# Kernel tuning notes

Measured on AMD Instinct MI355X. Metric: run time of the kernel, lower is better.

The kernel has to match this reference:

```python
import jax, jax.numpy as jnp
import numpy as np

IN_CHANNELS = 256


def setup_inputs() -> dict:
    key = jax.random.key(0)
    k0, k1, k2, k3 = jax.random.split(key, 4)
    N, C = 8192, IN_CHANNELS
    x = jax.random.normal(k0, (N, C), dtype=jnp.float32)
    # nn.Linear(C, C, bias=False): y = x @ W.T, W is [out, in] = [C, C]
    s = 1.0 / np.sqrt(C)
    Wq = jax.random.uniform(k1, (C, C), dtype=jnp.float32, minval=-s, maxval=s)
    Wk = jax.random.uniform(k2, (C, C), dtype=jnp.float32, minval=-s, maxval=s)
    Wv = jax.random.uniform(k3, (C, C), dtype=jnp.float32, minval=-s, maxval=s)
    return {"x": x, "Wq": Wq, "Wk": Wk, "Wv": Wv}


def reference(x, Wq, Wk, Wv):
    C = x.shape[-1]
    q = x @ Wq.T  # [N, C]
    k = x @ Wk.T  # [N, C]
    v = x @ Wv.T  # [N, C]
    scores = (q @ k.T) / jnp.sqrt(jnp.asarray(C, dtype=x.dtype))  # [N, N]
    attn = jax.nn.softmax(scores, axis=-1)
    return attn @ v  # [N, C]
```

## Files before the change

kernel.cpp:

```cpp
#include <hip/hip_runtime.h>
#include <hip/hip_bf16.h>


typedef short short8 __attribute__((ext_vector_type(8)));
typedef float f32x4 __attribute__((ext_vector_type(4)));
typedef float f32x16 __attribute__((ext_vector_type(16)));
typedef unsigned int u32x4 __attribute__((ext_vector_type(4)));

#define AS1 __attribute__((address_space(1)))
#define AS3 __attribute__((address_space(3)))

static __device__ __forceinline__ void gl_lds16(const void* g, void* l) {
    __builtin_amdgcn_global_load_lds((const AS1 unsigned int*)g,
                                     (AS3 unsigned int*)l, 16, 0, 0);
}

static __device__ __forceinline__ unsigned short f2bf(float f) {
    __hip_bfloat16 h = __float2bfloat16(f);
    return __builtin_bit_cast(unsigned short, h);
}
static __device__ __forceinline__ float bf2f(unsigned short u) {
    unsigned x = ((unsigned)u) << 16;
    return __builtin_bit_cast(float, x);
}
static __device__ __forceinline__ float exp2_fast(float x) {
    float r; asm("v_exp_f32 %0, %1" : "=v"(r) : "v"(x)); return r;
}
static __device__ __forceinline__ unsigned cvt_pk_bf16(float lo, float hi) {
    unsigned r;
    asm("v_cvt_pk_bf16_f32 %0, %1, %2" : "=v"(r) : "v"(lo), "v"(hi));
    return r;
}

static __device__ __forceinline__ short8 pack8(float4 a, float4 b) {
    short8 v;
    v[0] = (short)f2bf(a.x); v[1] = (short)f2bf(a.y);
    v[2] = (short)f2bf(a.z); v[3] = (short)f2bf(a.w);
    v[4] = (short)f2bf(b.x); v[5] = (short)f2bf(b.y);
    v[6] = (short)f2bf(b.z); v[7] = (short)f2bf(b.w);
    return v;
}

__global__ __launch_bounds__(256) void proj_kernel(
    const float* __restrict__ x, const float* __restrict__ Wq,
    const float* __restrict__ Wk, const float* __restrict__ Wv,
    unsigned short* __restrict__ qb, unsigned short* __restrict__ kbt,
    unsigned short* __restrict__ vtc)
{
    const int mb = blockIdx.x, nb = blockIdx.y;
    __shared__ unsigned short xs[64 * 256];
    __shared__ unsigned short wsh[64 * 256];
    const int tid = threadIdx.x;
    const int wid = tid >> 6, lane = tid & 63;
    const int l15 = lane & 15, kg = lane >> 4;

    for (int i = 0; i < 8; ++i) {
        int id = i * 256 + tid;
        int r = id >> 5, c = id & 31;
        {
            const float* g = x + (size_t)(mb * 64 + r) * 256 + c * 8;
            float4 f0 = *(const float4*)g, f1 = *(const float4*)(g + 4);
            *(short8*)&xs[r * 256 + ((c ^ (r & 7)) * 8)] = pack8(f0, f1);
        }
        {
            const float* g = Wq + (size_t)(nb * 64 + r) * 256 + c * 8;
            float4 f0 = *(const float4*)g, f1 = *(const float4*)(g + 4);
            *(short8*)&wsh[r * 256 + ((c ^ (r & 7)) * 8)] = pack8(f0, f1);
        }
    }
    __syncthreads();

    const int arow = wid * 16 + l15;
    short8 a[8];
#pragma unroll
    for (int ks = 0; ks < 8; ++ks)
        a[ks] = *(const short8*)&xs[arow * 256 + (((ks * 4 + kg) ^ (arow & 7)) * 8)];

    for (int w = 0; w < 3; ++w) {
        const float scale = (w == 0) ? 0.09016844005555f : 1.0f;
#pragma unroll
        for (int nt = 0; nt < 4; ++nt) {
            f32x4 acc = {0.f, 0.f, 0.f, 0.f};
            const int brow = nt * 16 + l15;
#pragma unroll
            for (int ks = 0; ks < 8; ++ks) {
                short8 b = *(const short8*)&wsh[brow * 256 + (((ks * 4 + kg) ^ (brow & 7)) * 8)];
                acc = __builtin_amdgcn_mfma_f32_16x16x32_bf16(a[ks], b, acc, 0, 0, 0);
            }
            const int gcol = nb * 64 + nt * 16 + l15;
#pragma unroll
            for (int r = 0; r < 4; ++r) {
                const int grow = mb * 64 + wid * 16 + kg * 4 + r;
                unsigned short h = f2bf(acc[r] * scale);
                if (w == 0) {
                    qb[(size_t)grow * 256 + gcol] = h;
                } else if (w == 1) {
                    kbt[(size_t)(grow >> 6) * 16384 + (gcol >> 3) * 512
                        + (grow & 63) * 8 + (gcol & 7)] = h;
                } else {
                    vtc[(size_t)(grow >> 3) * 2048 + (size_t)gcol * 8 + (grow & 7)] = h;
                }
            }
        }
        if (w < 2) {
            __syncthreads();
            const float* Wn = (w == 0) ? Wk : Wv;
            for (int i = 0; i < 8; ++i) {
                int id = i * 256 + tid;
                int r = id >> 5, c = id & 31;
                const float* g = Wn + (size_t)(nb * 64 + r) * 256 + c * 8;
                float4 f0 = *(const float4*)g, f1 = *(const float4*)(g + 4);
                *(short8*)&wsh[r * 256 + ((c ^ (r & 7)) * 8)] = pack8(f0, f1);
            }
            __syncthreads();
        }
    }
}

__global__ __launch_bounds__(512, 1) void attn_kernel(
    const unsigned short* __restrict__ qb, const unsigned short* __restrict__ kbt,
    const unsigned short* __restrict__ vtc,
    unsigned short* __restrict__ Opart, float* __restrict__ Mpart,
    float* __restrict__ Lpart)
{
    __shared__ unsigned short Ks[2][32 * 64 * 8];
    __shared__ unsigned short Vs[2][8 * 256 * 8];
    const int bid = blockIdx.x;
    const int split = bid & 7, qblk = bid >> 3;
    const int tid = threadIdx.x, wid = tid >> 6, lane = tid & 63;
    const int l31 = lane & 31, hi = lane >> 5;
    const int qrow0 = qblk * 256 + wid * 32;
    const int kv0 = split * 1024;

    short8 qf[16];
#pragma unroll
    for (int s = 0; s < 16; ++s)
        qf[s] = *(const short8*)(qb + (size_t)(qrow0 + l31) * 256 + s * 16 + hi * 8);

    f32x16 accO[8];
#pragma unroll
    for (int i = 0; i < 8; ++i) accO[i] = (f32x16)(0.f);
    f32x16 lacc = (f32x16)(0.f);
    float mrow = -1e30f;

    const int kbase_e = hi * 512 + l31 * 8;
    const int vbase_e = hi * 2048 + l31 * 8;

    auto stage = [&](int t, int b) {
        const size_t g = (size_t)(split * 16 + t);
        const unsigned short* ksrc = kbt + g * 16384 + lane * 8;
#pragma unroll
        for (int i = 0; i < 4; ++i) {
            const int cc = i * 8 + wid;
            gl_lds16(ksrc + cc * 512, &Ks[b][cc * 512]);
        }
        const size_t kcb = (size_t)(split * 128 + t * 8);
        const unsigned short* vsrc = vtc + kcb * 2048 + lane * 8;
#pragma unroll
        for (int i = 0; i < 4; ++i) {
            const int vi = i * 8 + wid;
            const int cc = vi >> 2, b64 = vi & 3;
            gl_lds16(vsrc + cc * 2048 + b64 * 512, &Vs[b][cc * 2048 + b64 * 512]);
        }
    };

    stage(0, 0);
    asm volatile("s_waitcnt vmcnt(0)" ::: "memory");
    __builtin_amdgcn_sched_barrier(0);
    __builtin_amdgcn_s_barrier();

    for (int t = 0; t < 16; ++t) {
        if (t < 15) stage(t + 1, (t + 1) & 1);

        const unsigned short* Kb = Ks[t & 1];
        const unsigned short* Vb = Vs[t & 1];

        f32x16 s0 = (f32x16)(0.f), s1 = (f32x16)(0.f);
        __builtin_amdgcn_s_setprio(1);
#pragma unroll
        for (int s = 0; s < 16; ++s) {
            short8 kf0 = *(const short8*)&Kb[kbase_e + s * 1024];
            short8 kf1 = *(const short8*)&Kb[kbase_e + s * 1024 + 256];
            s0 = __builtin_amdgcn_mfma_f32_32x32x16_bf16(kf0, qf[s], s0, 0, 0, 0);
            s1 = __builtin_amdgcn_mfma_f32_32x32x16_bf16(kf1, qf[s], s1, 0, 0, 0);
        }
        __builtin_amdgcn_s_setprio(0);

        float mt[16];
#pragma unroll
        for (int i = 0; i < 16; ++i) mt[i] = fmaxf(s0[i], s1[i]);
#pragma unroll
        for (int off = 8; off >= 1; off >>= 1)
#pragma unroll
            for (int i = 0; i < 8; ++i)
                if (i < off) mt[i] = fmaxf(mt[i], mt[i + off]);
        float mx = fmaxf(mt[0], __shfl_xor(mt[0], 32));

        if (!__all(mx <= mrow + 10.0f)) {
            const float mnew = fmaxf(mrow, mx);
            const float alpha = exp2_fast(mrow - mnew);
            float aR[16];
#pragma unroll
            for (int reg = 0; reg < 16; ++reg) {
                const int R = (reg & 3) + 8 * (reg >> 2) + 4 * hi;
                aR[reg] = __shfl(alpha, R);
            }
#pragma unroll
            for (int dt = 0; dt < 8; ++dt)
#pragma unroll
                for (int reg = 0; reg < 16; ++reg) accO[dt][reg] *= aR[reg];
            lacc = lacc * alpha;
            mrow = mnew;
        }
#pragma unroll
        for (int i = 0; i < 16; ++i) {
            s0[i] = exp2_fast(s0[i] - mrow);
            s1[i] = exp2_fast(s1[i] - mrow);
        }
        lacc = lacc + s0 + s1;

        short8 pa[4];
#pragma unroll
        for (int s = 0; s < 4; ++s) {
            const f32x16& P = (s >> 1) ? s1 : s0;
            const int q0 = 8 * (s & 1);
            unsigned X0 = cvt_pk_bf16(P[q0 + 0], P[q0 + 1]);
            unsigned X1 = cvt_pk_bf16(P[q0 + 2], P[q0 + 3]);
            unsigned Y0 = cvt_pk_bf16(P[q0 + 4], P[q0 + 5]);
            unsigned Y1 = cvt_pk_bf16(P[q0 + 6], P[q0 + 7]);
            asm volatile("v_permlane32_swap_b32 %0, %1" : "+v"(X0), "+v"(Y0));
            asm volatile("v_permlane32_swap_b32 %0, %1" : "+v"(X1), "+v"(Y1));
            u32x4 w = {X0, X1, Y0, Y1};
            pa[s] = __builtin_bit_cast(short8, w);
        }

        __builtin_amdgcn_s_setprio(1);
#pragma unroll
        for (int dt = 0; dt < 8; ++dt) {
            f32x16 acc = accO[dt];
#pragma unroll
            for (int s = 0; s < 4; ++s) {
                short8 vf = *(const short8*)&Vb[vbase_e + s * 4096 + dt * 256];
                acc = __builtin_amdgcn_mfma_f32_32x32x16_bf16(pa[s], vf, acc, 0, 0, 0);
            }
            accO[dt] = acc;
        }
        __builtin_amdgcn_s_setprio(0);

        asm volatile("s_waitcnt vmcnt(0)" ::: "memory");
        __builtin_amdgcn_sched_barrier(0);
        __builtin_amdgcn_s_barrier();
    }

    float lt[8];
#pragma unroll
    for (int i = 0; i < 8; ++i) lt[i] = lacc[i] + lacc[i + 8];
#pragma unroll
    for (int off = 4; off >= 1; off >>= 1)
#pragma unroll
        for (int i = 0; i < 4; ++i)
            if (i < off) lt[i] = lt[i] + lt[i + off];
    const float lrow = lt[0] + __shfl_xor(lt[0], 32);

#pragma unroll
    for (int dt = 0; dt < 8; ++dt) {
        const int d = dt * 32 + l31;
#pragma unroll
        for (int reg = 0; reg < 16; ++reg) {
            const int R = (reg & 3) + 8 * (reg >> 2) + 4 * hi;
            const int grow = qrow0 + R;
            Opart[((size_t)split * 8192 + grow) * 256 + d] = f2bf(accO[dt][reg]);
        }
    }
    if (hi == 0) {
        const int grow = qrow0 + l31;
        Mpart[split * 8192 + grow] = mrow;
        Lpart[split * 8192 + grow] = lrow;
    }
}

__global__ __launch_bounds__(256) void combine_kernel(
    const unsigned short* __restrict__ Opart, const float* __restrict__ Mpart,
    const float* __restrict__ Lpart, float* __restrict__ out)
{
    const int idx = blockIdx.x * 256 + threadIdx.x;
    const int row = idx >> 6;
    const int d = (idx & 63) * 4;
    float m[8], l[8];
#pragma unroll
    for (int s = 0; s < 8; ++s) {
        m[s] = Mpart[s * 8192 + row];
        l[s] = Lpart[s * 8192 + row];
    }
    float mm = m[0];
#pragma unroll
    for (int s = 1; s < 8; ++s) mm = fmaxf(mm, m[s]);
    float w[8], denom = 0.f;
#pragma unroll
    for (int s = 0; s < 8; ++s) { w[s] = exp2_fast(m[s] - mm); denom += l[s] * w[s]; }
    const float inv = 1.0f / denom;
    float4 acc = {0.f, 0.f, 0.f, 0.f};
#pragma unroll
    for (int s = 0; s < 8; ++s) {
        const unsigned short* p = Opart + ((size_t)s * 8192 + row) * 256 + d;
        unsigned long long u = *(const unsigned long long*)p;
        acc.x += bf2f((unsigned short)(u       & 0xffff)) * w[s];
        acc.y += bf2f((unsigned short)((u>>16) & 0xffff)) * w[s];
        acc.z += bf2f((unsigned short)((u>>32) & 0xffff)) * w[s];
        acc.w += bf2f((unsigned short)((u>>48) & 0xffff)) * w[s];
    }
    float4 r;
    r.x = acc.x * inv; r.y = acc.y * inv; r.z = acc.z * inv; r.w = acc.w * inv;
    *(float4*)(out + (size_t)row * 256 + d) = r;
}

extern "C" void kernel_launch(void* const* d_in, const int* in_sizes, int n_in,
                              void* d_out, int out_size, void* d_ws, size_t ws_size,
                              hipStream_t stream)
{
    const float* x  = (const float*)d_in[0];
    const float* Wq = (const float*)d_in[1];
    const float* Wk = (const float*)d_in[2];
    const float* Wv = (const float*)d_in[3];
    char* ws = (char*)d_ws;
    unsigned short* qb  = (unsigned short*)(ws);
    unsigned short* kbt = (unsigned short*)(ws + (4u << 20));
    unsigned short* vtc = (unsigned short*)(ws + (8u << 20));
    unsigned short* Opart = (unsigned short*)(ws + (12u << 20));
    float* Mpart = (float*)(ws + (44u << 20));
    float* Lpart = (float*)(ws + (44u << 20) + (1u << 18));
    float* out = (float*)d_out;

    dim3 gA(128, 4);
    proj_kernel<<<gA, 256, 0, stream>>>(x, Wq, Wk, Wv, qb, kbt, vtc);
    attn_kernel<<<256, 512, 0, stream>>>(qb, kbt, vtc, Opart, Mpart, Lpart);
    combine_kernel<<<2048, 256, 0, stream>>>(Opart, Mpart, Lpart, out);
}
```

Measured before the change: 105.4 us.

## Software-pipeline PV matmul one tile behind QK and split K/V staging

```diff
diff --git a/kernel.cpp b/kernel.cpp
--- a/kernel.cpp
+++ b/kernel.cpp
@@ -4,6 +4,7 @@
 
 typedef short short8 __attribute__((ext_vector_type(8)));
 typedef float f32x4 __attribute__((ext_vector_type(4)));
+typedef float f32x8 __attribute__((ext_vector_type(8)));
 typedef float f32x16 __attribute__((ext_vector_type(16)));
 typedef unsigned int u32x4 __attribute__((ext_vector_type(4)));
 
@@ -130,7 +131,6 @@
     const int tid = threadIdx.x, wid = tid >> 6, lane = tid & 63;
     const int l31 = lane & 31, hi = lane >> 5;
     const int qrow0 = qblk * 256 + wid * 32;
-    const int kv0 = split * 1024;
 
     short8 qf[16];
 #pragma unroll
@@ -140,13 +140,13 @@
     f32x16 accO[8];
 #pragma unroll
     for (int i = 0; i < 8; ++i) accO[i] = (f32x16)(0.f);
-    f32x16 lacc = (f32x16)(0.f);
+    f32x8 lacc = (f32x8)(0.f);
     float mrow = -1e30f;
 
     const int kbase_e = hi * 512 + l31 * 8;
     const int vbase_e = hi * 2048 + l31 * 8;
 
-    auto stage = [&](int t, int b) {
+    auto stageK = [&](int t, int b) {
         const size_t g = (size_t)(split * 16 + t);
         const unsigned short* ksrc = kbt + g * 16384 + lane * 8;
 #pragma unroll
@@ -154,6 +154,8 @@
             const int cc = i * 8 + wid;
             gl_lds16(ksrc + cc * 512, &Ks[b][cc * 512]);
         }
+    };
+    auto stageV = [&](int t, int b) {
         const size_t kcb = (size_t)(split * 128 + t * 8);
         const unsigned short* vsrc = vtc + kcb * 2048 + lane * 8;
 #pragma unroll
@@ -164,16 +166,18 @@
         }
     };
 
-    stage(0, 0);
+    stageK(0, 0);
     asm volatile("s_waitcnt vmcnt(0)" ::: "memory");
     __builtin_amdgcn_sched_barrier(0);
     __builtin_amdgcn_s_barrier();
 
+    short8 paO[4];
+
     for (int t = 0; t < 16; ++t) {
-        if (t < 15) stage(t + 1, (t + 1) & 1);
+        if (t < 15) stageK(t + 1, (t + 1) & 1);
+        stageV(t, t & 1);
 
         const unsigned short* Kb = Ks[t & 1];
-        const unsigned short* Vb = Vs[t & 1];
 
         f32x16 s0 = (f32x16)(0.f), s1 = (f32x16)(0.f);
         __builtin_amdgcn_s_setprio(1);
@@ -196,19 +200,11 @@
                 if (i < off) mt[i] = fmaxf(mt[i], mt[i + off]);
         float mx = fmaxf(mt[0], __shfl_xor(mt[0], 32));
 
-        if (!__all(mx <= mrow + 10.0f)) {
+        const bool resc = !__all(mx <= mrow + 10.0f);
+        float alpha = 1.0f;
+        if (resc) {
             const float mnew = fmaxf(mrow, mx);
-            const float alpha = exp2_fast(mrow - mnew);
-            float aR[16];
-#pragma unroll
-            for (int reg = 0; reg < 16; ++reg) {
-                const int R = (reg & 3) + 8 * (reg >> 2) + 4 * hi;
-                aR[reg] = __shfl(alpha, R);
-            }
-#pragma unroll
-            for (int dt = 0; dt < 8; ++dt)
-#pragma unroll
-                for (int reg = 0; reg < 16; ++reg) accO[dt][reg] *= aR[reg];
+            alpha = exp2_fast(mrow - mnew);
             lacc = lacc * alpha;
             mrow = mnew;
         }
@@ -217,9 +213,11 @@
             s0[i] = exp2_fast(s0[i] - mrow);
             s1[i] = exp2_fast(s1[i] - mrow);
         }
-        lacc = lacc + s0 + s1;
-
-        short8 pa[4];
+#pragma unroll
+        for (int i = 0; i < 8; ++i)
+            lacc[i] += (s0[i] + s0[i + 8]) + (s1[i] + s1[i + 8]);
+
+        short8 paN[4];
 #pragma unroll
         for (int s = 0; s < 4; ++s) {
             const f32x16& P = (s >> 1) ? s1 : s0;
@@ -231,30 +229,63 @@
             asm volatile("v_permlane32_swap_b32 %0, %1" : "+v"(X0), "+v"(Y0));
             asm volatile("v_permlane32_swap_b32 %0, %1" : "+v"(X1), "+v"(Y1));
             u32x4 w = {X0, X1, Y0, Y1};
-            pa[s] = __builtin_bit_cast(short8, w);
-        }
-
-        __builtin_amdgcn_s_setprio(1);
-#pragma unroll
-        for (int dt = 0; dt < 8; ++dt) {
-            f32x16 acc = accO[dt];
-#pragma unroll
-            for (int s = 0; s < 4; ++s) {
-                short8 vf = *(const short8*)&Vb[vbase_e + s * 4096 + dt * 256];
-                acc = __builtin_amdgcn_mfma_f32_32x32x16_bf16(pa[s], vf, acc, 0, 0, 0);
-            }
-            accO[dt] = acc;
-        }
-        __builtin_amdgcn_s_setprio(0);
+            paN[s] = __builtin_bit_cast(short8, w);
+        }
+
+        if (t > 0) {
+            const unsigned short* Vb = Vs[(t - 1) & 1];
+            __builtin_amdgcn_s_setprio(1);
+#pragma unroll
+            for (int dt = 0; dt < 8; ++dt) {
+                f32x16 acc = accO[dt];
+#pragma unroll
+                for (int s = 0; s < 4; ++s) {
+                    short8 vf = *(const short8*)&Vb[vbase_e + s * 4096 + dt * 256];
+                    acc = __builtin_amdgcn_mfma_f32_32x32x16_bf16(paO[s], vf, acc, 0, 0, 0);
+                }
+                accO[dt] = acc;
+            }
+            __builtin_amdgcn_s_setprio(0);
+        }
+
+        if (resc) {
+            float aR[16];
+#pragma unroll
+            for (int reg = 0; reg < 16; ++reg) {
+                const int R = (reg & 3) + 8 * (reg >> 2) + 4 * hi;
+                aR[reg] = __shfl(alpha, R);
+            }
+#pragma unroll
+            for (int dt = 0; dt < 8; ++dt)
+#pragma unroll
+                for (int reg = 0; reg < 16; ++reg) accO[dt][reg] *= aR[reg];
+        }
+
+#pragma unroll
+        for (int s = 0; s < 4; ++s) paO[s] = paN[s];
 
         asm volatile("s_waitcnt vmcnt(0)" ::: "memory");
         __builtin_amdgcn_sched_barrier(0);
         __builtin_amdgcn_s_barrier();
     }
 
+    {
+        const unsigned short* Vb = Vs[15 & 1];
+#pragma unroll
+        for (int dt = 0; dt < 8; ++dt) {
+            f32x16 acc = accO[dt];
+#pragma unroll
+            for (int s = 0; s < 4; ++s) {
+                short8 vf = *(const short8*)&Vb[vbase_e + s * 4096 + dt * 256];
+                acc = __builtin_amdgcn_mfma_f32_32x32x16_bf16(paO[s], vf, acc, 0, 0, 0);
+            }
+            accO[dt] = acc;
+        }
+    }
+
     float lt[8];
 #pragma unroll
-    for (int i = 0; i < 8; ++i) lt[i] = lacc[i] + lacc[i + 8];
+    for (int i = 0; i < 8; ++i) lt[i] = lacc[i];
 #pragma unroll
     for (int off = 4; off >= 1; off >>= 1)
 #pragma unroll
```

After: 109.0 us. +3.4%, slower.
